# Optimization experiments

Measured on AMD Instinct MI355X. Metric: run time of the kernel, lower is better.

Reference implementation:

```python
import jax, jax.numpy as jnp
import numpy as np
import math

D = 1024
H = 16
DH = D // H


def sinusoidal_pe(length, d):
    pos = jnp.arange(length, dtype=jnp.float32)[:, None]            # [S,1]
    div = jnp.exp(jnp.arange(0, d, 2, dtype=jnp.float32) * (-math.log(10000.0) / d))  # [d/2]
    ang = pos * div                                                  # [S,d/2]
    # interleave sin (even idx) and cos (odd idx)
    return jnp.stack([jnp.sin(ang), jnp.cos(ang)], axis=-1).reshape(length, d)


def setup_inputs() -> dict:
    key = jax.random.key(0)
    ks = jax.random.split(key, 12)
    s = 0.02
    x = jax.random.normal(ks[0], (2, 2048, D), dtype=jnp.float32)
    return {
        "x": x,
        "ln_g": jnp.ones((D,), jnp.float32),
        "ln_b": jnp.zeros((D,), jnp.float32),
        "Wq": jax.random.normal(ks[1], (D, D), jnp.float32) * s,
        "bq": jnp.zeros((D,), jnp.float32),
        "Wk": jax.random.normal(ks[2], (D, D), jnp.float32) * s,
        "bk": jnp.zeros((D,), jnp.float32),
        "Wv": jax.random.normal(ks[3], (D, D), jnp.float32) * s,
        "bv": jnp.zeros((D,), jnp.float32),
        "Wp": jax.random.normal(ks[4], (D, D), jnp.float32) * s,
        "Wo": jax.random.normal(ks[5], (D, D), jnp.float32) * s,
        "bo": jnp.zeros((D,), jnp.float32),
        "u_bias": jax.random.normal(ks[6], (H, DH), jnp.float32) * 0.05,
        "v_bias": jax.random.normal(ks[7], (H, DH), jnp.float32) * 0.05,
    }


def _relative_shift(pos_score):
    # pos_score: [B,H,S,S]
    B, Hh, S1, S2 = pos_score.shape
    padded = jnp.concatenate([jnp.zeros((B, Hh, S1, 1), pos_score.dtype), pos_score], axis=-1)
    padded = padded.reshape(B, Hh, S2 + 1, S1)
    return padded[:, :, 1:].reshape(B, Hh, S1, S2)


def reference(x, ln_g, ln_b, Wq, bq, Wk, bk, Wv, bv, Wp, Wo, bo, u_bias, v_bias):
    B, S, Dm = x.shape
    dh = Dm // H
    scale = dh ** -0.5

    pe = sinusoidal_pe(S, Dm)                                        # [S,D]

    mu = jnp.mean(x, axis=-1, keepdims=True)
    var = jnp.var(x, axis=-1, keepdims=True)
    xn = (x - mu) / jnp.sqrt(var + 1e-5) * ln_g + ln_b

    q = (xn @ Wq + bq).reshape(B, S, H, dh)                          # [B,S,H,dh]
    k = (xn @ Wk + bk).reshape(B, S, H, dh)
    v = (xn @ Wv + bv).reshape(B, S, H, dh)
    p = (pe @ Wp).reshape(S, H, dh)                                  # [S,H,dh]

    content = jnp.einsum('bihd,bjhd->bhij', q + u_bias, k)
    pos = jnp.einsum('bihd,jhd->bhij', q + v_bias, p)
    pos = _relative_shift(pos)

    attn = jax.nn.softmax((content + pos) * scale, axis=-1)          # [B,H,S,S]
    head = jnp.einsum('bhij,bjhd->bihd', attn, v).reshape(B, S, Dm)
    return head @ Wo + bo
```

## Files before the change

### kernel.cpp

```cpp
#include <hip/hip_runtime.h>
#include <hip/hip_bf16.h>
#include <math.h>

#define Dm   1024
#define Hh   16
#define Sx   2048

typedef short s16x8 __attribute__((ext_vector_type(8)));
typedef float f32x4 __attribute__((ext_vector_type(4)));
typedef unsigned short u16;
typedef u16 u16x4 __attribute__((ext_vector_type(4)));

#if defined(__has_builtin)
#  if __has_builtin(__builtin_amdgcn_cvt_pk_bf16_f32)
#    define HAVE_PKBF16 1
typedef __bf16 bfv2 __attribute__((ext_vector_type(2)));
#  endif
#  if __has_builtin(__builtin_amdgcn_exp2f)
#    define EXP2(x) __builtin_amdgcn_exp2f(x)
#  endif
#endif
#ifndef EXP2
#  define EXP2(x) exp2f(x)
#endif

#define ATT_SCALE 0.1803368801111204f

__device__ __forceinline__ float wave_sum64(float v) {
#pragma unroll
    for (int o = 32; o > 0; o >>= 1) v += __shfl_xor(v, o, 64);
    return v;
}
__device__ __forceinline__ u16 f2bf(float x) {
    unsigned int u = __float_as_uint(x);
    unsigned int r = u + 0x7FFFu + ((u >> 16) & 1u);
    return (u16)(r >> 16);
}
__device__ __forceinline__ float bf2f(u16 h) {
    return __uint_as_float(((unsigned int)h) << 16);
}
__device__ __forceinline__ f32x4 mfma16(s16x8 a, s16x8 b, f32x4 c) {
    return __builtin_amdgcn_mfma_f32_16x16x32_bf16(a, b, c, 0, 0, 0);
}

__global__ __launch_bounds__(256) void ln_kernel(const float* __restrict__ x,
                                                 const float* __restrict__ g,
                                                 const float* __restrict__ b,
                                                 u16* __restrict__ out16) {
    int row = blockIdx.x;
    int tid = threadIdx.x;
    const float4* xr = (const float4*)(x + (size_t)row * Dm);
    float4 v = xr[tid];
    float s  = v.x + v.y + v.z + v.w;
    float ss = v.x * v.x + v.y * v.y + v.z * v.z + v.w * v.w;
    __shared__ float rbuf[8];
    s  = wave_sum64(s);
    ss = wave_sum64(ss);
    if ((tid & 63) == 0) { rbuf[tid >> 6] = s; rbuf[4 + (tid >> 6)] = ss; }
    __syncthreads();
    float mean = (rbuf[0] + rbuf[1] + rbuf[2] + rbuf[3]) * (1.0f / Dm);
    float msq  = (rbuf[4] + rbuf[5] + rbuf[6] + rbuf[7]) * (1.0f / Dm);
    float var  = msq - mean * mean;
    float rstd = 1.0f / sqrtf(var + 1e-5f);
    float4 gg = ((const float4*)g)[tid];
    float4 bb = ((const float4*)b)[tid];
    float o[4];
    o[0] = (v.x - mean) * rstd * gg.x + bb.x;
    o[1] = (v.y - mean) * rstd * gg.y + bb.y;
    o[2] = (v.z - mean) * rstd * gg.z + bb.z;
    o[3] = (v.w - mean) * rstd * gg.w + bb.w;
    u16x4 hi, lo;
#pragma unroll
    for (int i = 0; i < 4; i++) {
        u16 h = f2bf(o[i]);
        hi[i] = h;
        lo[i] = f2bf(o[i] - bf2f(h));
    }
    *(u16x4*)&out16[(size_t)row * 2048 + tid * 4]        = hi;
    *(u16x4*)&out16[(size_t)row * 2048 + 1024 + tid * 4] = lo;
}

__global__ __launch_bounds__(256) void pe_kernel(u16* __restrict__ pe16) {
    int idx = blockIdx.x * 256 + threadIdx.x;
    int r = idx >> 9;
    int t = idx & 511;
    double div = exp((double)(2 * t) * (-9.210340371976184 / 1024.0));
    double ang = (double)r * div;
    float sv = (float)sin(ang), cv = (float)cos(ang);
    u16 sh = f2bf(sv), chh = f2bf(cv);
    u16* row = pe16 + (size_t)r * 2048;
    row[2 * t]            = sh;
    row[2 * t + 1]        = chh;
    row[1024 + 2 * t]     = f2bf(sv - bf2f(sh));
    row[1024 + 2 * t + 1] = f2bf(cv - bf2f(chh));
}

__global__ __launch_bounds__(256) void wconv_kernel(const float* __restrict__ W0,
                                                    const float* __restrict__ W1,
                                                    const float* __restrict__ W2,
                                                    const float* __restrict__ W3,
                                                    const float* __restrict__ W4,
                                                    u16* __restrict__ WT) {
    int wz = blockIdx.z;
    const float* W = (wz == 0) ? W0 : (wz == 1) ? W1 : (wz == 2) ? W2 : (wz == 3) ? W3 : W4;
    u16* T = WT + (size_t)wz * 1024 * 2048;
    __shared__ float tile[32][33];
    int n0 = blockIdx.x * 32, k0 = blockIdx.y * 32;
    int tx = threadIdx.x & 31, ty = threadIdx.x >> 5;
#pragma unroll
    for (int r = 0; r < 32; r += 8)
        tile[ty + r][tx] = W[(size_t)(k0 + ty + r) * 1024 + n0 + tx];
    __syncthreads();
#pragma unroll
    for (int r = 0; r < 32; r += 8) {
        int n = ty + r;
        float x = tile[tx][n];
        u16 h = f2bf(x);
        float rem = x - bf2f(h);
        T[(size_t)(n0 + n) * 2048 + k0 + tx]        = h;
        T[(size_t)(n0 + n) * 2048 + 1024 + k0 + tx] = f2bf(rem);
    }
}

__global__ __launch_bounds__(256, 3) void gemm128(const u16* __restrict__ A,
                                                  const u16* __restrict__ A2,
                                                  const u16* __restrict__ WT,
                                                  const float* __restrict__ b0,
                                                  const float* __restrict__ b1,
                                                  const float* __restrict__ b2,
                                                  u16* __restrict__ Cb,
                                                  float* __restrict__ C,
                                                  int mode) {
    __shared__ __align__(16) u16 Ah[128 * 72];
    __shared__ __align__(16) u16 Bh[128 * 72];
    int tid = threadIdx.x;
    int gx, gy, widx;
    const u16* Asrc = A;
    if (mode == 0) {
        int bid = blockIdx.x;
        if (bid < 768) { gx = bid % 24; gy = bid / 24; widx = gx >> 3; gx &= 7; }
        else           { int r2 = bid - 768; gx = r2 & 7; gy = r2 >> 3; widx = 3; Asrc = A2; }
    } else {
        gx = blockIdx.x; gy = blockIdx.y; widx = 4;
    }
    int bn = gx * 128, bm = gy * 128;
    const u16* Wb = WT + (size_t)widx * (1024 * 2048);
    const float* bias = (widx == 0) ? b0 : (widx == 1) ? b1 : (widx == 2) ? b2
                      : (widx == 4) ? b0 : nullptr;
    float csc = (widx == 1 || widx == 3) ? ATT_SCALE : 1.0f;

    int w = tid >> 6, ln = tid & 63, g = ln >> 4, l15 = ln & 15;
    int wm = (w & 1) * 64, wn = (w >> 1) * 64;

    int srow = tid >> 3, c8 = tid & 7;
    int half = c8 >> 2, cIn = c8 & 3;
    const u16* Agp = Asrc + (size_t)(bm + srow) * 2048 + half * 1024 + cIn * 8;
    const u16* Bgp = Wb   + (size_t)(bn + srow) * 2048 + half * 1024 + cIn * 8;
    u16* Aw = &Ah[srow * 72 + half * 32 + cIn * 8];
    u16* Bw = &Bh[srow * 72 + half * 32 + cIn * 8];

    f32x4 acc[4][4] = {};

    s16x8 pa0 = *(const s16x8*)(Agp);
    s16x8 pa1 = *(const s16x8*)(Agp + 65536);
    s16x8 pa2 = *(const s16x8*)(Agp + 131072);
    s16x8 pa3 = *(const s16x8*)(Agp + 196608);
    s16x8 pb0 = *(const s16x8*)(Bgp);
    s16x8 pb1 = *(const s16x8*)(Bgp + 65536);
    s16x8 pb2 = *(const s16x8*)(Bgp + 131072);
    s16x8 pb3 = *(const s16x8*)(Bgp + 196608);

    for (int k0 = 0; k0 < 1024; k0 += 32) {
        __syncthreads();
        *(s16x8*)(Aw)           = pa0;
        *(s16x8*)(Aw + 32 * 72) = pa1;
        *(s16x8*)(Aw + 64 * 72) = pa2;
        *(s16x8*)(Aw + 96 * 72) = pa3;
        *(s16x8*)(Bw)           = pb0;
        *(s16x8*)(Bw + 32 * 72) = pb1;
        *(s16x8*)(Bw + 64 * 72) = pb2;
        *(s16x8*)(Bw + 96 * 72) = pb3;
        int kn = k0 + 32;
        pa0 = *(const s16x8*)(Agp + kn);
        pa1 = *(const s16x8*)(Agp + 65536 + kn);
        pa2 = *(const s16x8*)(Agp + 131072 + kn);
        pa3 = *(const s16x8*)(Agp + 196608 + kn);
        pb0 = *(const s16x8*)(Bgp + kn);
        pb1 = *(const s16x8*)(Bgp + 65536 + kn);
        pb2 = *(const s16x8*)(Bgp + 131072 + kn);
        pb3 = *(const s16x8*)(Bgp + 196608 + kn);
        __syncthreads();

        s16x8 bhf[4], blf[4];
#pragma unroll
        for (int nt = 0; nt < 4; nt++) {
            int br = (wn + nt * 16 + l15) * 72;
            bhf[nt] = *(const s16x8*)&Bh[br + g * 8];
            blf[nt] = *(const s16x8*)&Bh[br + 32 + g * 8];
        }
#pragma unroll
        for (int mt = 0; mt < 4; mt++) {
            int ar = (wm + mt * 16 + l15) * 72;
            s16x8 ah = *(const s16x8*)&Ah[ar + g * 8];
            s16x8 al = *(const s16x8*)&Ah[ar + 32 + g * 8];
#pragma unroll
            for (int nt = 0; nt < 4; nt++) {
                acc[mt][nt] = mfma16(ah, bhf[nt], acc[mt][nt]);
                acc[mt][nt] = mfma16(al, bhf[nt], acc[mt][nt]);
                acc[mt][nt] = mfma16(ah, blf[nt], acc[mt][nt]);
            }
        }
    }

    float bv4[4];
#pragma unroll
    for (int nt = 0; nt < 4; nt++)
        bv4[nt] = bias ? bias[bn + wn + nt * 16 + l15] : 0.0f;
    if (mode == 0) {
        u16* Co = Cb + (size_t)widx * (4096 * 1024);
#pragma unroll
        for (int mt = 0; mt < 4; mt++)
#pragma unroll
            for (int r = 0; r < 4; r++) {
                int row = bm + wm + mt * 16 + g * 4 + r;
                u16* cp = Co + (size_t)row * 1024 + bn + wn + l15;
#pragma unroll
                for (int nt = 0; nt < 4; nt++)
                    cp[16 * nt] = f2bf((acc[mt][nt][r] + bv4[nt]) * csc);
            }
    } else {
#pragma unroll
        for (int mt = 0; mt < 4; mt++)
#pragma unroll
            for (int r = 0; r < 4; r++) {
                int row = bm + wm + mt * 16 + g * 4 + r;
                float* cp = C + (size_t)row * 1024 + bn + wn + l15;
#pragma unroll
                for (int nt = 0; nt < 4; nt++)
                    cp[16 * nt] = acc[mt][nt][r] + bv4[nt];
            }
    }
}

__global__ __launch_bounds__(256) void vtrans_kernel(const u16* __restrict__ v,
                                                     u16* __restrict__ vT) {
    __shared__ u16 L[32 * 72];
    int jt = blockIdx.x, h = blockIdx.y, b = blockIdx.z;
    int tid = threadIdx.x;
    int row = tid >> 3, cc = tid & 7;
    const u16* src = v + ((size_t)(b * Sx + jt * 32 + row)) * Dm + h * 64 + cc * 8;
    *(s16x8*)&L[row * 72 + cc * 8] = *(const s16x8*)src;
    __syncthreads();
    int d = tid >> 2, jq = tid & 3;
    s16x8 o;
#pragma unroll
    for (int jj = 0; jj < 8; jj++) o[jj] = (short)L[(jq * 8 + jj) * 72 + d];
    u16* dst = vT + (((size_t)(b * 16 + h) * 64 + jt)) * 2048 + d * 32 + jq * 8;
    *(s16x8*)dst = o;
}

__global__ __launch_bounds__(256) void ukvb_kernel(const u16* __restrict__ k,
                                                   const u16* __restrict__ pp,
                                                   const float* __restrict__ u,
                                                   const float* __restrict__ vb,
                                                   float* __restrict__ ukg,
                                                   float* __restrict__ vbg) {
    int jid = blockIdx.x * 256 + threadIdx.x;
    const u16* src; const float* vec; float* dst; int idx;
    if (jid < 2 * Hh * Sx) {
        int j = jid & 2047, h = (jid >> 11) & 15, b = jid >> 15;
        src = k + ((size_t)(b * Sx + j)) * Dm + h * 64;
        vec = u + h * 64; dst = ukg; idx = jid;
    } else {
        int j2 = jid - 2 * Hh * Sx;
        int r = j2 & 2047, h = j2 >> 11;
        src = pp + (size_t)r * Dm + h * 64;
        vec = vb + h * 64; dst = vbg; idx = j2;
    }
    float s = 0.0f;
#pragma unroll
    for (int c = 0; c < 8; c++) {
        s16x8 kk = *(const s16x8*)(src + c * 8);
#pragma unroll
        for (int i = 0; i < 8; i++) s += bf2f((u16)kk[i]) * vec[c * 8 + i];
    }
    dst[idx] = s;
}

__device__ __forceinline__ void wfill2(s16x8 a0, s16x8 a1, const u16* PW,
                                       int g, int l15, f32x4& d0, f32x4& d1) {
    f32x4 z = {0.f, 0.f, 0.f, 0.f};
    s16x8 b00 = *(const s16x8*)&PW[l15 * 72 + g * 8];
    s16x8 b01 = *(const s16x8*)&PW[l15 * 72 + 32 + g * 8];
    s16x8 b10 = *(const s16x8*)&PW[(16 + l15) * 72 + g * 8];
    s16x8 b11 = *(const s16x8*)&PW[(16 + l15) * 72 + 32 + g * 8];
    d0 = __builtin_amdgcn_mfma_f32_16x16x32_bf16(a0, b00, z, 0, 0, 0);
    d0 = __builtin_amdgcn_mfma_f32_16x16x32_bf16(a1, b01, d0, 0, 0, 0);
    d1 = __builtin_amdgcn_mfma_f32_16x16x32_bf16(a0, b10, z, 0, 0, 0);
    d1 = __builtin_amdgcn_mfma_f32_16x16x32_bf16(a1, b11, d1, 0, 0, 0);
}

__device__ __forceinline__ void window_fill(s16x8 aq0, s16x8 aq1, s16x8 ab0, s16x8 ab1,
                                            const u16* PW, float* Ws,
                                            const float* __restrict__ vbb,
                                            int vstart, int sb, int rbase, int g, int l15) {
    f32x4 e0, e1;
    if (vstart + 31 <= Sx) {
        wfill2(aq0, aq1, PW, g, l15, e0, e1);
    } else if (vstart > Sx) {
        wfill2(ab0, ab1, PW, g, l15, e0, e1);
    } else {
        f32x4 d0, d1, f0, f1;
        wfill2(aq0, aq1, PW, g, l15, d0, d1);
        wfill2(ab0, ab1, PW, g, l15, f0, f1);
        int v0 = vstart + l15, v1 = vstart + 16 + l15;
#pragma unroll
        for (int r = 0; r < 4; r++) {
            e0[r] = (v0 > Sx) ? f0[r] : d0[r];
            e1[r] = (v1 > Sx) ? f1[r] : d1[r];
        }
    }
    int v0 = vstart + l15, v1 = vstart + 16 + l15;
    int pc0 = v0 < Sx ? v0 : v0 - Sx - 1;
    int pc1 = v1 < Sx ? v1 : v1 - Sx - 1;
    float vb0 = (v0 == Sx) ? 0.0f : vbb[pc0];
    float vb1 = (v1 == Sx) ? 0.0f : vbb[pc1];
    int bs = sb + rbase;
#pragma unroll
    for (int r = 0; r < 4; r++) {
        int b2 = bs + r; if (b2 >= 96) b2 -= 96;
        int sl0 = b2 + l15; if (sl0 >= 96) sl0 -= 96;
        int sl1 = sl0 + 16; if (sl1 >= 96) sl1 -= 96;
        Ws[(rbase + r) * 98 + sl0] = (v0 == Sx) ? 0.0f : e0[r] + vb0;
        Ws[(rbase + r) * 98 + sl1] = (v1 == Sx) ? 0.0f : e1[r] + vb1;
    }
}

__global__ __launch_bounds__(256, 4) void flash_kernel(const u16* __restrict__ q,
                                                       const u16* __restrict__ k,
                                                       const u16* __restrict__ vt,
                                                       const u16* __restrict__ pp,
                                                       const float* __restrict__ ukg,
                                                       const float* __restrict__ vbg,
                                                       u16* __restrict__ head16) {
    __shared__ __align__(16) unsigned char smem[39424];
    float* Ws = (float*)smem;
    u16*   Qs = (u16*)smem;
    u16*   Kt = (u16*)(smem + 25088);
    u16*   PW = (u16*)(smem + 29696);
    u16*   PA = (u16*)(smem + 34304);

    int tid = threadIdx.x, blk = blockIdx.x;
    int grp = (blk & 7) + 8 * (blk >> 8);
    int it  = (blk >> 3) & 31;
    int h = grp & 15, b = grp >> 4;
    int i0 = it * 64;
    int a0 = 1984 - i0;

    const u16* qb  = q  + ((size_t)b * Sx) * Dm + h * 64;
    const u16* kb  = k  + ((size_t)b * Sx) * Dm + h * 64;
    const u16* vtb = vt + ((size_t)(b * 16 + h) * 64) * 2048;
    const u16* ppb = pp + h * 64;
    const float* ukb = ukg + (size_t)(b * Hh + h) * Sx;
    const float* vbb = vbg + (size_t)h * Sx;

    int w = tid >> 6, ln = tid & 63, g = ln >> 4, l15 = ln & 15;
    int rv = tid >> 3, ch = tid & 7;
    int rbase = 16 * w + 4 * g;

    for (int c = tid; c < 65 * 8; c += 256) {
        int row = c >> 3, cc = c & 7;
        int i = i0 + row;
        s16x8 tv = {0, 0, 0, 0, 0, 0, 0, 0};
        if (i < Sx) tv = *(const s16x8*)(qb + (size_t)i * Dm + cc * 8);
        *(s16x8*)&Qs[row * 72 + cc * 8] = tv;
    }
    __syncthreads();

    s16x8 aq0 = *(const s16x8*)&Qs[(16 * w + l15) * 72 + g * 8];
    s16x8 aq1 = *(const s16x8*)&Qs[(16 * w + l15) * 72 + 32 + g * 8];
    s16x8 ab0 = *(const s16x8*)&Qs[(16 * w + 1 + l15) * 72 + g * 8];
    s16x8 ab1 = *(const s16x8*)&Qs[(16 * w + 1 + l15) * 72 + 32 + g * 8];
    __syncthreads();

    for (int f = 0; f < 3; f++) {
        int vrb = f * 32;
        if (f) __syncthreads();
        {
            int vv = a0 + vrb + rv;
            s16x8 tv = {0, 0, 0, 0, 0, 0, 0, 0};
            if (vv != Sx) {
                int pc = vv < Sx ? vv : vv - Sx - 1;
                tv = *(const s16x8*)(ppb + (size_t)pc * Dm + ch * 8);
            }
            *(s16x8*)&PW[rv * 72 + ch * 8] = tv;
        }
        __syncthreads();
        window_fill(aq0, aq1, ab0, ab1, PW, Ws, vbb, a0 + vrb, vrb, rbase, g, l15);
    }

    f32x4 O[4] = {{0.f,0.f,0.f,0.f},{0.f,0.f,0.f,0.f},{0.f,0.f,0.f,0.f},{0.f,0.f,0.f,0.f}};
    float m_w = -1e30f;
    float l_i[4] = {0.f, 0.f, 0.f, 0.f};
    int wro[4];
#pragma unroll
    for (int r = 0; r < 4; r++) wro[r] = (rbase + r) * 98;
    int sb = 0;
    int jm = 63;
    int cw = (g >= 2) ? 16 : 0;
    int crd = (l15 >> 3) << 4;
    int pard = (16 * w + l15) * 40 + ((g * 8 + crd) & 31);

    const u16* pK = kb + (size_t)rv * Dm + ch * 8;
    const u16* pV = vtb + l15 * 32 + g * 8;
    s16x8 rK = *(const s16x8*)pK;
    s16x8 rPW = {0, 0, 0, 0, 0, 0, 0, 0};

    for (int t = 0; t < 64; t++) {
        int j0 = t * 32;
        __syncthreads();
        *(s16x8*)&Kt[rv * 72 + ch * 8] = rK;
        if (t >= 1) *(s16x8*)&PW[rv * 72 + ch * 8] = rPW;

        s16x8 bv0 = *(const s16x8*)(pV);
        s16x8 bv1 = *(const s16x8*)(pV + 512);
        s16x8 bv2 = *(const s16x8*)(pV + 1024);
        s16x8 bv3 = *(const s16x8*)(pV + 1536);
        pV += 2048;

        pK += 32 * Dm;
        rK = *(const s16x8*)pK;
        {
            int vv = a0 + (t + 3) * 32 + rv;
            s16x8 z8 = {0, 0, 0, 0, 0, 0, 0, 0};
            if (vv != Sx) {
                int pc = vv < Sx ? vv : vv - Sx - 1;
                if (pc > Sx - 1) pc = Sx - 1;
                z8 = *(const s16x8*)(ppb + (size_t)pc * Dm + ch * 8);
            }
            rPW = z8;
        }
        float uk0 = ukb[j0 + l15];
        float uk1 = ukb[j0 + 16 + l15];
        __syncthreads();

        f32x4 s0, s1;
        {
            f32x4 z = {0.f, 0.f, 0.f, 0.f};
            s16x8 bk00 = *(const s16x8*)&Kt[l15 * 72 + g * 8];
            s16x8 bk01 = *(const s16x8*)&Kt[l15 * 72 + 32 + g * 8];
            s16x8 bk10 = *(const s16x8*)&Kt[(16 + l15) * 72 + g * 8];
            s16x8 bk11 = *(const s16x8*)&Kt[(16 + l15) * 72 + 32 + g * 8];
            s0 = __builtin_amdgcn_mfma_f32_16x16x32_bf16(aq0, bk00, z, 0, 0, 0);
            s0 = __builtin_amdgcn_mfma_f32_16x16x32_bf16(aq1, bk01, s0, 0, 0, 0);
            s1 = __builtin_amdgcn_mfma_f32_16x16x32_bf16(aq0, bk10, z, 0, 0, 0);
            s1 = __builtin_amdgcn_mfma_f32_16x16x32_bf16(aq1, bk11, s1, 0, 0, 0);
        }

        if (t >= 1) {
            window_fill(aq0, aq1, ab0, ab1, PW, Ws, vbb, a0 + j0 + 64, sb, rbase, g, l15);
            sb += 32; if (sb >= 96) sb -= 96;
        }

        int si0 = jm + l15; if (si0 >= 96) si0 -= 96;
        int si1 = si0 + 16; if (si1 >= 96) si1 -= 96;
        jm += 32; if (jm >= 96) jm -= 96;
        float lg0[4], lg1[4];
#pragma unroll
        for (int r = 0; r < 4; r++) {
            lg0[r] = s0[r] + uk0 + Ws[wro[r] + si0];
            lg1[r] = s1[r] + uk1 + Ws[wro[r] + si1];
        }
        float pmax = fmaxf(fmaxf(fmaxf(lg0[0], lg1[0]), fmaxf(lg0[1], lg1[1])),
                           fmaxf(fmaxf(lg0[2], lg1[2]), fmaxf(lg0[3], lg1[3])));
        if (__any(pmax > m_w + 8.0f)) {
            float mx = pmax;
#pragma unroll
            for (int o = 1; o < 64; o <<= 1) mx = fmaxf(mx, __shfl_xor(mx, o, 64));
            float alpha = EXP2(m_w - mx);
            m_w = mx;
            l_i[0] *= alpha; l_i[1] *= alpha; l_i[2] *= alpha; l_i[3] *= alpha;
#pragma unroll
            for (int nt = 0; nt < 4; nt++)
#pragma unroll
                for (int r = 0; r < 4; r++) O[nt][r] *= alpha;
        }
        int c0 = l15 + cw;
        int c1 = l15 + 16 - cw;
#pragma unroll
        for (int r = 0; r < 4; r++) {
            float e0v = EXP2(lg0[r] - m_w);
            float e1v = EXP2(lg1[r] - m_w);
            l_i[r] += e0v + e1v;
#ifdef HAVE_PKBF16
            bfv2 pk2 = __builtin_amdgcn_cvt_pk_bf16_f32(e0v, e1v);
            PA[(rbase + r) * 40 + c0] = __builtin_bit_cast(u16, pk2[0]);
            PA[(rbase + r) * 40 + c1] = __builtin_bit_cast(u16, pk2[1]);
#else
            PA[(rbase + r) * 40 + c0] = f2bf(e0v);
            PA[(rbase + r) * 40 + c1] = f2bf(e1v);
#endif
        }

        {
            s16x8 ap = *(const s16x8*)&PA[pard];
            O[0] = __builtin_amdgcn_mfma_f32_16x16x32_bf16(ap, bv0, O[0], 0, 0, 0);
            O[1] = __builtin_amdgcn_mfma_f32_16x16x32_bf16(ap, bv1, O[1], 0, 0, 0);
            O[2] = __builtin_amdgcn_mfma_f32_16x16x32_bf16(ap, bv2, O[2], 0, 0, 0);
            O[3] = __builtin_amdgcn_mfma_f32_16x16x32_bf16(ap, bv3, O[3], 0, 0, 0);
        }
    }

#pragma unroll
    for (int r = 0; r < 4; r++) {
        float l = l_i[r];
#pragma unroll
        for (int o = 1; o < 16; o <<= 1) l += __shfl_xor(l, o, 64);
        float inv = 1.0f / l;
        int grow = i0 + rbase + r;
        u16* dst = head16 + (size_t)(b * Sx + grow) * 2048 + h * 64 + l15;
#pragma unroll
        for (int nt = 0; nt < 4; nt++) {
            float f = O[nt][r] * inv;
            u16 hh = f2bf(f);
            dst[16 * nt]        = hh;
            dst[1024 + 16 * nt] = f2bf(f - bf2f(hh));
        }
    }
}

extern "C" void kernel_launch(void* const* d_in, const int* in_sizes, int n_in,
                              void* d_out, int out_size, void* d_ws, size_t ws_size,
                              hipStream_t stream) {
    const float* x    = (const float*)d_in[0];
    const float* ln_g = (const float*)d_in[1];
    const float* ln_b = (const float*)d_in[2];
    const float* Wq   = (const float*)d_in[3];
    const float* bq   = (const float*)d_in[4];
    const float* Wk   = (const float*)d_in[5];
    const float* bk   = (const float*)d_in[6];
    const float* Wv   = (const float*)d_in[7];
    const float* bv   = (const float*)d_in[8];
    const float* Wp   = (const float*)d_in[9];
    const float* Wo   = (const float*)d_in[10];
    const float* bo   = (const float*)d_in[11];
    const float* ub   = (const float*)d_in[12];
    const float* vbias= (const float*)d_in[13];

    float* out = (float*)d_out;
    u16* base  = (u16*)d_ws;

    const int MROWS = 2 * Sx;
    u16* xn16   = base;
    u16* head16 = base + 8u  * 1024 * 1024;
    u16* pe16   = base + 16u * 1024 * 1024;
    u16* qb16   = base + 20u * 1024 * 1024;
    u16* kb16   = base + 24u * 1024 * 1024;
    u16* vb16   = base + 28u * 1024 * 1024;
    u16* pp16   = base + 32u * 1024 * 1024;
    u16* vT16   = base + 34u * 1024 * 1024;
    u16* WT     = base + 38u * 1024 * 1024;
    float* ukg  = (float*)(base + 48u * 1024 * 1024);
    float* vbg  = ukg + 2 * Hh * Sx;

    ln_kernel<<<MROWS, 256, 0, stream>>>(x, ln_g, ln_b, xn16);
    pe_kernel<<<Sx * 512 / 256, 256, 0, stream>>>(pe16);

    dim3 gw(32, 32, 5);
    wconv_kernel<<<gw, 256, 0, stream>>>(Wq, Wk, Wv, Wp, Wo, WT);

    gemm128<<<896, 256, 0, stream>>>(xn16, pe16, WT, bq, bk, bv, qb16, nullptr, 0);

    dim3 gv(Sx / 32, Hh, 2);
    vtrans_kernel<<<gv, 256, 0, stream>>>(vb16, vT16);

    ukvb_kernel<<<(2 * Hh * Sx + Hh * Sx) / 256, 256, 0, stream>>>(kb16, pp16, ub, vbias, ukg, vbg);

    flash_kernel<<<2 * Hh * 32, 256, 0, stream>>>(qb16, kb16, vT16, pp16, ukg, vbg, head16);

    gemm128<<<dim3(8, 32), 256, 0, stream>>>(head16, nullptr, WT, bo, nullptr, nullptr, nullptr, out, 1);
}
```

Before: 405.3 us.

## Use direct global-to-LDS loads with XOR swizzle in projection GEMMs

The GEMM kernel now copies A/B tiles straight from global memory into LDS with global_load_lds, replacing register prefetch plus LDS stores. An XOR-swizzled unpadded layout replaces the padded one to avoid bank conflicts. The kernel is templated on tile height, and the output projection uses 64-row tiles to launch more blocks, with the occupancy hint raised to 4. Register double-buffering is gone, so global latency is no longer hidden behind the previous tile's MFMAs, and each iteration now carries a load-then-sync-then-compute dependency.

```diff
diff --git a/kernel.cpp b/kernel.cpp
--- a/kernel.cpp
+++ b/kernel.cpp
@@ -41,6 +41,11 @@
 }
 __device__ __forceinline__ f32x4 mfma16(s16x8 a, s16x8 b, f32x4 c) {
     return __builtin_amdgcn_mfma_f32_16x16x32_bf16(a, b, c, 0, 0, 0);
+}
+__device__ __forceinline__ void gl16(const u16* gp, u16* lp) {
+    __builtin_amdgcn_global_load_lds(
+        (__attribute__((address_space(1))) void*)(gp),
+        (__attribute__((address_space(3))) void*)(lp), 16, 0, 0);
 }
 
 __global__ __launch_bounds__(256) void ln_kernel(const float* __restrict__ x,
@@ -122,17 +127,21 @@
     }
 }
 
-__global__ __launch_bounds__(256, 3) void gemm128(const u16* __restrict__ A,
-                                                  const u16* __restrict__ A2,
-                                                  const u16* __restrict__ WT,
-                                                  const float* __restrict__ b0,
-                                                  const float* __restrict__ b1,
-                                                  const float* __restrict__ b2,
-                                                  u16* __restrict__ Cb,
-                                                  float* __restrict__ C,
-                                                  int mode) {
-    __shared__ __align__(16) u16 Ah[128 * 72];
-    __shared__ __align__(16) u16 Bh[128 * 72];
+template<int BMT>
+__global__ __launch_bounds__(256, 4) void gemm128k(const u16* __restrict__ A,
+                                                   const u16* __restrict__ A2,
+                                                   const u16* __restrict__ WT,
+                                                   const float* __restrict__ b0,
+                                                   const float* __restrict__ b1,
+                                                   const float* __restrict__ b2,
+                                                   u16* __restrict__ Cb,
+                                                   float* __restrict__ C,
+                                                   int mode) {
+    constexpr int MT  = BMT / 32;
+    constexpr int AC  = BMT / 32;
+    constexpr int RPW = BMT / 4;
+    __shared__ __align__(16) u16 AhL[BMT * 64];
+    __shared__ __align__(16) u16 BhL[128 * 64];
     int tid = threadIdx.x;
     int gx, gy, widx;
     const u16* Asrc = A;
@@ -143,66 +152,50 @@
     } else {
         gx = blockIdx.x; gy = blockIdx.y; widx = 4;
     }
-    int bn = gx * 128, bm = gy * 128;
+    int bn = gx * 128, bm = gy * BMT;
     const u16* Wb = WT + (size_t)widx * (1024 * 2048);
     const float* bias = (widx == 0) ? b0 : (widx == 1) ? b1 : (widx == 2) ? b2
                       : (widx == 4) ? b0 : nullptr;
     float csc = (widx == 1 || widx == 3) ? ATT_SCALE : 1.0f;
 
     int w = tid >> 6, ln = tid & 63, g = ln >> 4, l15 = ln & 15;
-    int wm = (w & 1) * 64, wn = (w >> 1) * 64;
-
-    int srow = tid >> 3, c8 = tid & 7;
-    int half = c8 >> 2, cIn = c8 & 3;
-    const u16* Agp = Asrc + (size_t)(bm + srow) * 2048 + half * 1024 + cIn * 8;
-    const u16* Bgp = Wb   + (size_t)(bn + srow) * 2048 + half * 1024 + cIn * 8;
-    u16* Aw = &Ah[srow * 72 + half * 32 + cIn * 8];
-    u16* Bw = &Bh[srow * 72 + half * 32 + cIn * 8];
-
-    f32x4 acc[4][4] = {};
-
-    s16x8 pa0 = *(const s16x8*)(Agp);
-    s16x8 pa1 = *(const s16x8*)(Agp + 65536);
-    s16x8 pa2 = *(const s16x8*)(Agp + 131072);
-    s16x8 pa3 = *(const s16x8*)(Agp + 196608);
-    s16x8 pb0 = *(const s16x8*)(Bgp);
-    s16x8 pb1 = *(const s16x8*)(Bgp + 65536);
-    s16x8 pb2 = *(const s16x8*)(Bgp + 131072);
-    s16x8 pb3 = *(const s16x8*)(Bgp + 196608);
+    int wm = (w & 1) * (BMT / 2), wn = (w >> 1) * 64;
+
+    int key = ln >> 3;
+    int cg  = (ln & 7) ^ key;
+    int gcol = (cg < 4) ? cg * 8 : 1024 + (cg - 4) * 8;
+    const u16* gA = Asrc + (size_t)(bm + w * RPW + key) * 2048 + gcol;
+    const u16* gB = Wb   + (size_t)(bn + w * 32  + key) * 2048 + gcol;
+    u16* lA = &AhL[(w * RPW) * 64];
+    u16* lB = &BhL[(w * 32) * 64];
+
+    int keyr = l15 & 7;
+    int chH = (g ^ keyr) * 8;
+    int chL = ((4 + g) ^ keyr) * 8;
+
+    f32x4 acc[MT][4] = {};
 
     for (int k0 = 0; k0 < 1024; k0 += 32) {
+#pragma unroll
+        for (int c = 0; c < AC; c++)
+            gl16(gA + c * (8 * 2048) + k0, lA + c * (8 * 64));
+#pragma unroll
+        for (int c = 0; c < 4; c++)
+            gl16(gB + c * (8 * 2048) + k0, lB + c * (8 * 64));
         __syncthreads();
-        *(s16x8*)(Aw)           = pa0;
-        *(s16x8*)(Aw + 32 * 72) = pa1;
-        *(s16x8*)(Aw + 64 * 72) = pa2;
-        *(s16x8*)(Aw + 96 * 72) = pa3;
-        *(s16x8*)(Bw)           = pb0;
-        *(s16x8*)(Bw + 32 * 72) = pb1;
-        *(s16x8*)(Bw + 64 * 72) = pb2;
-        *(s16x8*)(Bw + 96 * 72) = pb3;
-        int kn = k0 + 32;
-        pa0 = *(const s16x8*)(Agp + kn);
-        pa1 = *(const s16x8*)(Agp + 65536 + kn);
-        pa2 = *(const s16x8*)(Agp + 131072 + kn);
-        pa3 = *(const s16x8*)(Agp + 196608 + kn);
-        pb0 = *(const s16x8*)(Bgp + kn);
-        pb1 = *(const s16x8*)(Bgp + 65536 + kn);
-        pb2 = *(const s16x8*)(Bgp + 131072 + kn);
-        pb3 = *(const s16x8*)(Bgp + 196608 + kn);
-        __syncthreads();
 
         s16x8 bhf[4], blf[4];
 #pragma unroll
         for (int nt = 0; nt < 4; nt++) {
-            int br = (wn + nt * 16 + l15) * 72;
-            bhf[nt] = *(const s16x8*)&Bh[br + g * 8];
-            blf[nt] = *(const s16x8*)&Bh[br + 32 + g * 8];
-        }
-#pragma unroll
-        for (int mt = 0; mt < 4; mt++) {
-            int ar = (wm + mt * 16 + l15) * 72;
-            s16x8 ah = *(const s16x8*)&Ah[ar + g * 8];
-            s16x8 al = *(const s16x8*)&Ah[ar + 32 + g * 8];
+            int br = (wn + nt * 16 + l15) * 64;
+            bhf[nt] = *(const s16x8*)&BhL[br + chH];
+            blf[nt] = *(const s16x8*)&BhL[br + chL];
+        }
+#pragma unroll
+        for (int mt = 0; mt < MT; mt++) {
+            int ar = (wm + mt * 16 + l15) * 64;
+            s16x8 ah = *(const s16x8*)&AhL[ar + chH];
+            s16x8 al = *(const s16x8*)&AhL[ar + chL];
 #pragma unroll
             for (int nt = 0; nt < 4; nt++) {
                 acc[mt][nt] = mfma16(ah, bhf[nt], acc[mt][nt]);
@@ -210,6 +203,7 @@
                 acc[mt][nt] = mfma16(ah, blf[nt], acc[mt][nt]);
             }
         }
+        __syncthreads();
     }
 
     float bv4[4];
@@ -219,7 +213,7 @@
     if (mode == 0) {
         u16* Co = Cb + (size_t)widx * (4096 * 1024);
 #pragma unroll
-        for (int mt = 0; mt < 4; mt++)
+        for (int mt = 0; mt < MT; mt++)
 #pragma unroll
             for (int r = 0; r < 4; r++) {
                 int row = bm + wm + mt * 16 + g * 4 + r;
@@ -230,7 +224,7 @@
             }
     } else {
 #pragma unroll
-        for (int mt = 0; mt < 4; mt++)
+        for (int mt = 0; mt < MT; mt++)
 #pragma unroll
             for (int r = 0; r < 4; r++) {
                 int row = bm + wm + mt * 16 + g * 4 + r;
@@ -569,7 +563,7 @@
     dim3 gw(32, 32, 5);
     wconv_kernel<<<gw, 256, 0, stream>>>(Wq, Wk, Wv, Wp, Wo, WT);
 
-    gemm128<<<896, 256, 0, stream>>>(xn16, pe16, WT, bq, bk, bv, qb16, nullptr, 0);
+    gemm128k<128><<<896, 256, 0, stream>>>(xn16, pe16, WT, bq, bk, bv, qb16, nullptr, 0);
 
     dim3 gv(Sx / 32, Hh, 2);
     vtrans_kernel<<<gv, 256, 0, stream>>>(vb16, vT16);
@@ -578,5 +572,5 @@
 
     flash_kernel<<<2 * Hh * 32, 256, 0, stream>>>(qb16, kb16, vT16, pp16, ukg, vbg, head16);
 
-    gemm128<<<dim3(8, 32), 256, 0, stream>>>(head16, nullptr, WT, bo, nullptr, nullptr, nullptr, out, 1);
-}
+    gemm128k<64><<<dim3(8, 64), 256, 0, stream>>>(head16, nullptr, WT, bo, nullptr, nullptr, nullptr, out, 1);
+}
```

Result: faster. 387.0 us (-4.5%).
